# Kernel optimization log

Hardware: AMD Instinct MI355X
Metric: run time of the kernel (lower is better)

Reference implementation:

```python
import jax, jax.numpy as jnp
import numpy as np

B, T, I = 16384, 50, 5
H = 128
PRED_LEN = 12


def _uniform(key, shape, bound):
    return jax.random.uniform(key, shape, jnp.float32, -bound, bound)


def setup_inputs() -> dict:
    key = jax.random.key(0)
    ks = jax.random.split(key, 12)
    bound = 1.0 / np.sqrt(H)  # PyTorch LSTM/Linear default init
    return {
        "x": jax.random.normal(ks[0], (B, T, I), jnp.float32),
        "enc_Wih": _uniform(ks[1], (4 * H, I), bound),
        "enc_Whh": _uniform(ks[2], (4 * H, H), bound),
        "enc_bih": _uniform(ks[3], (4 * H,), bound),
        "enc_bhh": _uniform(ks[4], (4 * H,), bound),
        "dec_Wih": _uniform(ks[5], (4 * H, I), bound),
        "dec_Whh": _uniform(ks[6], (4 * H, H), bound),
        "dec_bih": _uniform(ks[7], (4 * H,), bound),
        "dec_bhh": _uniform(ks[8], (4 * H,), bound),
        "lin_W": _uniform(ks[9], (2, H), bound),
        "lin_b": _uniform(ks[10], (2,), bound),
    }


def _lstm_cell(x_t, h, c, Wih, Whh, bih, bhh):
    # PyTorch gate order: i, f, g, o
    gates = x_t @ Wih.T + h @ Whh.T + (bih + bhh)  # [B, 4H]
    i, f, g, o = jnp.split(gates, 4, axis=-1)
    i = jax.nn.sigmoid(i)
    f = jax.nn.sigmoid(f)
    g = jnp.tanh(g)
    o = jax.nn.sigmoid(o)
    c_new = f * c + i * g
    h_new = o * jnp.tanh(c_new)
    return h_new, c_new


def reference(x, enc_Wih, enc_Whh, enc_bih, enc_bhh,
              dec_Wih, dec_Whh, dec_bih, dec_bhh, lin_W, lin_b):
    b = x.shape[0]
    h0 = jnp.zeros((b, H), x.dtype)
    c0 = jnp.zeros((b, H), x.dtype)

    # ---- encoder LSTM over the history sequence ----
    def enc_step(carry, x_t):
        h, c = carry
        h, c = _lstm_cell(x_t, h, c, enc_Wih, enc_Whh, enc_bih, enc_bhh)
        return (h, c), None

    (h, c), _ = jax.lax.scan(enc_step, (h0, c0), jnp.swapaxes(x, 0, 1))

    static_context = x[:, -1, 2:]          # [B, I-2]
    last_velocity = x[:, -1, :2]           # [B, 2]
    dec_in0 = jnp.concatenate([last_velocity, static_context], axis=1)  # [B, I]

    def dec_step(carry, _):
        h, c, dec_in = carry
        h, c = _lstm_cell(dec_in, h, c, dec_Wih, dec_Whh, dec_bih, dec_bhh)
        pred = h @ lin_W.T + lin_b                      # [B, 2]
        dec_in = jnp.concatenate([pred, static_context], axis=1)
        return (h, c, dec_in), pred

    _, preds = jax.lax.scan(dec_step, (h, c, dec_in0), None, length=PRED_LEN)
    return jnp.swapaxes(preds, 0, 1)  # [B, pred_len, 2]
```

## Files before the change

kernel.cpp:

```cpp
#include <hip/hip_runtime.h>
#include <cstdint>

#define TT 50
#define II 5
#define PRED 12

typedef _Float16 f16;
typedef _Float16 f16x8 __attribute__((ext_vector_type(8)));
typedef float f32x4 __attribute__((ext_vector_type(4)));

__global__ void prep_weights(const float* __restrict__ Wih, const float* __restrict__ Whh,
                             const float* __restrict__ bih, const float* __restrict__ bhh,
                             f16* __restrict__ outw) {
    int f = blockIdx.x * 256 + threadIdx.x;
    if (f >= 81920) return;
    int j  = f & 7;
    int c  = (f >> 3) & 15;
    int q  = (f >> 7) & 3;
    int t2 = f >> 9;
    int kc = t2 % 5;
    int wg = t2 / 5;
    int w = wg >> 2, gsub = wg & 3;
    int g = gsub * 128 + w * 16 + c;
    int k = kc * 32 + q * 8 + j;
    float v;
    if (k < 128)       v = Whh[g * 128 + k];
    else if (k < 133)  v = Wih[g * 5 + (k - 128)];
    else if (k == 133) v = bih[g] + bhh[g];
    else               v = 0.f;
    outw[f] = (f16)v;
}

__device__ __forceinline__ float fsig(float x) {
    return __builtin_amdgcn_rcpf(1.f + __builtin_amdgcn_exp2f(-1.4426950408889634f * x));
}
__device__ __forceinline__ float ftanh(float x) {
    return 1.f - 2.f * __builtin_amdgcn_rcpf(1.f + __builtin_amdgcn_exp2f(2.885390081777927f * x));
}

__global__ __launch_bounds__(512, 2)
void lstm_kernel(const float* __restrict__ x,
                 const f16* __restrict__ wfrag,
                 const float* __restrict__ linW, const float* __restrict__ linB,
                 float* __restrict__ out) {
    __shared__ __align__(16) unsigned char state[64 * 512];
    __shared__ float predpart[8][64][2];

    const int tid  = threadIdx.x;
    const int lane = tid & 63;
    const int w    = tid >> 6;
    const int q    = lane >> 4;
    const int cl   = lane & 15;
    const int s0   = blockIdx.x * 64;
    const int jb   = w * 16 + q * 4;
    const int physh = ((jb >> 3) ^ (2 * cl)) & 31;
    const int hoff  = (jb & 7) * 2;

    f16x8 wr[4][5];
    {
        const f16x8* wp = (const f16x8*)wfrag;
        #pragma unroll
        for (int gs = 0; gs < 4; ++gs) {
            #pragma unroll
            for (int kc = 0; kc < 5; ++kc)
                wr[gs][kc] = wp[((w * 4 + gs) * 5 + kc) * 64 + lane];
        }
    }
    float w0r[4], w1r[4];
    #pragma unroll
    for (int idx = 0; idx < 4; ++idx) {
        w0r[idx] = linW[jb + idx];
        w1r[idx] = linW[128 + jb + idx];
    }
    float sc0 = 0.f, sc1 = 0.f, sc2 = 0.f;
    if (tid < 64) {
        const float* xr = x + (size_t)(s0 + tid) * (TT * II) + 49 * II;
        sc0 = xr[2]; sc1 = xr[3]; sc2 = xr[4];
    }
    {
        uint32_t* sp = (uint32_t*)state;
        #pragma unroll
        for (int r = 0; r < 16; ++r) sp[tid + r * 512] = 0u;
    }
    float creg[4][4];
    #pragma unroll
    for (int a = 0; a < 4; ++a)
        #pragma unroll
        for (int b = 0; b < 4; ++b) creg[a][b] = 0.f;

    __syncthreads();
    if (tid < 64) {
        const float* xr = x + (size_t)(s0 + tid) * (TT * II);
        union { f16 h[8]; uint4 u; } pk;
        pk.h[0] = (f16)xr[0]; pk.h[1] = (f16)xr[1]; pk.h[2] = (f16)xr[2];
        pk.h[3] = (f16)xr[3]; pk.h[4] = (f16)xr[4];
        pk.h[5] = (f16)1.f; pk.h[6] = (f16)0.f; pk.h[7] = (f16)0.f;
        int phys = 16 ^ (2 * (tid & 15));
        *(uint4*)(state + tid * 512 + phys * 16) = pk.u;
    }
    __syncthreads();

    f32x4 zero4 = {0.f, 0.f, 0.f, 0.f};

    #pragma unroll 1
    for (int t = 0; t < TT; ++t) {
        float xv0 = 0, xv1 = 0, xv2 = 0, xv3 = 0, xv4 = 0;
        if (tid < 64) {
            int tn = (t < TT - 1) ? t + 1 : TT - 1;
            const float* xr = x + (size_t)(s0 + tid) * (TT * II) + tn * II;
            xv0 = xr[0]; xv1 = xr[1]; xv2 = xr[2]; xv3 = xr[3]; xv4 = xr[4];
        }
        f32x4 acc[4][4];
        #pragma unroll
        for (int gs = 0; gs < 4; ++gs)
            #pragma unroll
            for (int ns = 0; ns < 4; ++ns) acc[gs][ns] = zero4;

        #pragma unroll
        for (int ns = 0; ns < 4; ++ns) {
            const int srow = ns * 16 + cl;
            #pragma unroll
            for (int kc = 0; kc < 5; ++kc) {
                const int phys = (kc * 4 + q) ^ (2 * cl);
                f16x8 bf = *(const f16x8*)(state + srow * 512 + phys * 16);
                acc[0][ns] = __builtin_amdgcn_mfma_f32_16x16x32_f16(wr[0][kc], bf, acc[0][ns], 0, 0, 0);
                acc[1][ns] = __builtin_amdgcn_mfma_f32_16x16x32_f16(wr[1][kc], bf, acc[1][ns], 0, 0, 0);
                acc[2][ns] = __builtin_amdgcn_mfma_f32_16x16x32_f16(wr[2][kc], bf, acc[2][ns], 0, 0, 0);
                acc[3][ns] = __builtin_amdgcn_mfma_f32_16x16x32_f16(wr[3][kc], bf, acc[3][ns], 0, 0, 0);
            }
        }
        uint2 hp[4];
        #pragma unroll
        for (int ns = 0; ns < 4; ++ns) {
            union { f16 h[4]; uint2 u; } pk;
            #pragma unroll
            for (int idx = 0; idx < 4; ++idx) {
                float ii = fsig(acc[0][ns][idx]);
                float ff = fsig(acc[1][ns][idx]);
                float gg = ftanh(acc[2][ns][idx]);
                float oo = fsig(acc[3][ns][idx]);
                float cn = ff * creg[ns][idx] + ii * gg;
                creg[ns][idx] = cn;
                pk.h[idx] = (f16)(oo * ftanh(cn));
            }
            hp[ns] = pk.u;
        }
        __syncthreads();
        #pragma unroll
        for (int ns = 0; ns < 4; ++ns)
            *(uint2*)(state + (ns * 16 + cl) * 512 + physh * 16 + hoff) = hp[ns];
        if (tid < 64) {
            union { f16 h[8]; uint4 u; } pk;
            pk.h[0] = (f16)xv0; pk.h[1] = (f16)xv1; pk.h[2] = (f16)xv2;
            pk.h[3] = (f16)xv3; pk.h[4] = (f16)xv4;
            pk.h[5] = (f16)1.f; pk.h[6] = (f16)0.f; pk.h[7] = (f16)0.f;
            int phys = 16 ^ (2 * (tid & 15));
            *(uint4*)(state + tid * 512 + phys * 16) = pk.u;
        }
        __syncthreads();
    }

    {
        const f16x8* wp = (const f16x8*)(wfrag + 81920);
        #pragma unroll
        for (int gs = 0; gs < 4; ++gs) {
            #pragma unroll
            for (int kc = 0; kc < 5; ++kc)
                wr[gs][kc] = wp[((w * 4 + gs) * 5 + kc) * 64 + lane];
        }
    }

    #pragma unroll 1
    for (int td = 0; td < PRED; ++td) {
        f32x4 acc[4][4];
        #pragma unroll
        for (int gs = 0; gs < 4; ++gs)
            #pragma unroll
            for (int ns = 0; ns < 4; ++ns) acc[gs][ns] = zero4;

        #pragma unroll
        for (int ns = 0; ns < 4; ++ns) {
            const int srow = ns * 16 + cl;
            #pragma unroll
            for (int kc = 0; kc < 5; ++kc) {
                const int phys = (kc * 4 + q) ^ (2 * cl);
                f16x8 bf = *(const f16x8*)(state + srow * 512 + phys * 16);
                acc[0][ns] = __builtin_amdgcn_mfma_f32_16x16x32_f16(wr[0][kc], bf, acc[0][ns], 0, 0, 0);
                acc[1][ns] = __builtin_amdgcn_mfma_f32_16x16x32_f16(wr[1][kc], bf, acc[1][ns], 0, 0, 0);
                acc[2][ns] = __builtin_amdgcn_mfma_f32_16x16x32_f16(wr[2][kc], bf, acc[2][ns], 0, 0, 0);
                acc[3][ns] = __builtin_amdgcn_mfma_f32_16x16x32_f16(wr[3][kc], bf, acc[3][ns], 0, 0, 0);
            }
        }
        uint2 hp[4];
        float p0[4], p1[4];
        #pragma unroll
        for (int ns = 0; ns < 4; ++ns) {
            union { f16 h[4]; uint2 u; } pk;
            p0[ns] = 0.f; p1[ns] = 0.f;
            #pragma unroll
            for (int idx = 0; idx < 4; ++idx) {
                float ii = fsig(acc[0][ns][idx]);
                float ff = fsig(acc[1][ns][idx]);
                float gg = ftanh(acc[2][ns][idx]);
                float oo = fsig(acc[3][ns][idx]);
                float cn = ff * creg[ns][idx] + ii * gg;
                creg[ns][idx] = cn;
                float hv = oo * ftanh(cn);
                p0[ns] += hv * w0r[idx];
                p1[ns] += hv * w1r[idx];
                pk.h[idx] = (f16)hv;
            }
            hp[ns] = pk.u;
        }
        #pragma unroll
        for (int ns = 0; ns < 4; ++ns) {
            p0[ns] += __shfl_xor(p0[ns], 16);
            p0[ns] += __shfl_xor(p0[ns], 32);
            p1[ns] += __shfl_xor(p1[ns], 16);
            p1[ns] += __shfl_xor(p1[ns], 32);
        }
        if (q == 0) {
            #pragma unroll
            for (int ns = 0; ns < 4; ++ns) {
                predpart[w][ns * 16 + cl][0] = p0[ns];
                predpart[w][ns * 16 + cl][1] = p1[ns];
            }
        }
        __syncthreads();
        #pragma unroll
        for (int ns = 0; ns < 4; ++ns)
            *(uint2*)(state + (ns * 16 + cl) * 512 + physh * 16 + hoff) = hp[ns];
        if (tid < 64) {
            float a0 = linB[0], a1 = linB[1];
            #pragma unroll
            for (int ww = 0; ww < 8; ++ww) {
                a0 += predpart[ww][tid][0];
                a1 += predpart[ww][tid][1];
            }
            float2 o2; o2.x = a0; o2.y = a1;
            *(float2*)(out + (size_t)(s0 + tid) * (PRED * 2) + td * 2) = o2;
            union { f16 h[8]; uint4 u; } pk;
            pk.h[0] = (f16)a0; pk.h[1] = (f16)a1;
            pk.h[2] = (f16)sc0; pk.h[3] = (f16)sc1; pk.h[4] = (f16)sc2;
            pk.h[5] = (f16)1.f; pk.h[6] = (f16)0.f; pk.h[7] = (f16)0.f;
            int phys = 16 ^ (2 * (tid & 15));
            *(uint4*)(state + tid * 512 + phys * 16) = pk.u;
        }
        __syncthreads();
    }
}

extern "C" void kernel_launch(void* const* d_in, const int* in_sizes, int n_in,
                              void* d_out, int out_size, void* d_ws, size_t ws_size,
                              hipStream_t stream) {
    (void)in_sizes; (void)n_in; (void)out_size; (void)ws_size;
    const float* x    = (const float*)d_in[0];
    const float* eWih = (const float*)d_in[1];
    const float* eWhh = (const float*)d_in[2];
    const float* ebih = (const float*)d_in[3];
    const float* ebhh = (const float*)d_in[4];
    const float* dWih = (const float*)d_in[5];
    const float* dWhh = (const float*)d_in[6];
    const float* dbih = (const float*)d_in[7];
    const float* dbhh = (const float*)d_in[8];
    const float* linW = (const float*)d_in[9];
    const float* linB = (const float*)d_in[10];
    f16* wfrag = (f16*)d_ws;

    prep_weights<<<320, 256, 0, stream>>>(eWih, eWhh, ebih, ebhh, wfrag);
    prep_weights<<<320, 256, 0, stream>>>(dWih, dWhh, dbih, dbhh, wfrag + 81920);
    lstm_kernel<<<256, 512, 0, stream>>>(x, wfrag, linW, linB, (float*)d_out);
}
```

Measured before the change: 279.5 us.

## Halve samples per block, double-buffer hidden state, stage x in LDS, drop prep kernels

Each block now handles 32 samples instead of 64 and the grid doubles to 512, with launch bounds raised to 4 blocks per CU, so more blocks can be resident across the device. The hidden state is double-buffered in LDS, which removes one barrier per timestep. All x inputs are staged as f16 in LDS up front instead of being loaded from global memory every step. The two weight-prep kernels are removed and each block converts the fp32 weights to f16 fragments itself, trading extra redundant global reads per block for fewer launches. The x/bias input chunk now goes through a separate MFMA operand, and the smaller per-block tile gives less weight reuse per block.

```diff
diff --git a/kernel.cpp b/kernel.cpp
--- a/kernel.cpp
+++ b/kernel.cpp
@@ -4,33 +4,13 @@
 #define TT 50
 #define II 5
 #define PRED 12
+#define SAMP 32
+#define NSB 2
 
 typedef _Float16 f16;
 typedef _Float16 f16x8 __attribute__((ext_vector_type(8)));
 typedef float f32x4 __attribute__((ext_vector_type(4)));
 
-__global__ void prep_weights(const float* __restrict__ Wih, const float* __restrict__ Whh,
-                             const float* __restrict__ bih, const float* __restrict__ bhh,
-                             f16* __restrict__ outw) {
-    int f = blockIdx.x * 256 + threadIdx.x;
-    if (f >= 81920) return;
-    int j  = f & 7;
-    int c  = (f >> 3) & 15;
-    int q  = (f >> 7) & 3;
-    int t2 = f >> 9;
-    int kc = t2 % 5;
-    int wg = t2 / 5;
-    int w = wg >> 2, gsub = wg & 3;
-    int g = gsub * 128 + w * 16 + c;
-    int k = kc * 32 + q * 8 + j;
-    float v;
-    if (k < 128)       v = Whh[g * 128 + k];
-    else if (k < 133)  v = Wih[g * 5 + (k - 128)];
-    else if (k == 133) v = bih[g] + bhh[g];
-    else               v = 0.f;
-    outw[f] = (f16)v;
-}
-
 __device__ __forceinline__ float fsig(float x) {
     return __builtin_amdgcn_rcpf(1.f + __builtin_amdgcn_exp2f(-1.4426950408889634f * x));
 }
@@ -38,200 +18,210 @@
     return 1.f - 2.f * __builtin_amdgcn_rcpf(1.f + __builtin_amdgcn_exp2f(2.885390081777927f * x));
 }
 
-__global__ __launch_bounds__(512, 2)
+__device__ __forceinline__ void load_frags(const float* __restrict__ Wih,
+                                           const float* __restrict__ Whh,
+                                           const float* __restrict__ bih,
+                                           const float* __restrict__ bhh,
+                                           int w, int q, int cl, f16x8 wr[4][5]) {
+    #pragma unroll
+    for (int gs = 0; gs < 4; ++gs) {
+        const int g = gs * 128 + w * 16 + cl;
+        const float* whr = Whh + g * 128 + q * 8;
+        #pragma unroll
+        for (int kc = 0; kc < 4; ++kc) {
+            f32x4 a = *(const f32x4*)(whr + kc * 32);
+            f32x4 b = *(const f32x4*)(whr + kc * 32 + 4);
+            f16x8 f;
+            f[0] = (f16)a[0]; f[1] = (f16)a[1]; f[2] = (f16)a[2]; f[3] = (f16)a[3];
+            f[4] = (f16)b[0]; f[5] = (f16)b[1]; f[6] = (f16)b[2]; f[7] = (f16)b[3];
+            wr[gs][kc] = f;
+        }
+        f16x8 f;
+        #pragma unroll
+        for (int j = 0; j < 8; ++j) f[j] = (f16)0.f;
+        if (q == 0) {
+            f[0] = (f16)Wih[g * 5 + 0]; f[1] = (f16)Wih[g * 5 + 1];
+            f[2] = (f16)Wih[g * 5 + 2]; f[3] = (f16)Wih[g * 5 + 3];
+            f[4] = (f16)Wih[g * 5 + 4];
+            f[5] = (f16)(bih[g] + bhh[g]);
+        }
+        wr[gs][4] = f;
+    }
+}
+
+__global__ __launch_bounds__(512, 4)
 void lstm_kernel(const float* __restrict__ x,
-                 const f16* __restrict__ wfrag,
+                 const float* __restrict__ eWih, const float* __restrict__ eWhh,
+                 const float* __restrict__ ebih, const float* __restrict__ ebhh,
+                 const float* __restrict__ dWih, const float* __restrict__ dWhh,
+                 const float* __restrict__ dbih, const float* __restrict__ dbhh,
                  const float* __restrict__ linW, const float* __restrict__ linB,
                  float* __restrict__ out) {
-    __shared__ __align__(16) unsigned char state[64 * 512];
-    __shared__ float predpart[8][64][2];
+    __shared__ __align__(16) unsigned char state[2 * SAMP * 256];
+    __shared__ __align__(16) f16 xstage[52 * SAMP * 8];
+    __shared__ float predpart[8][SAMP][2];
 
     const int tid  = threadIdx.x;
     const int lane = tid & 63;
     const int w    = tid >> 6;
     const int q    = lane >> 4;
     const int cl   = lane & 15;
-    const int s0   = blockIdx.x * 64;
+    const int s0   = blockIdx.x * SAMP;
     const int jb   = w * 16 + q * 4;
-    const int physh = ((jb >> 3) ^ (2 * cl)) & 31;
+    const int physh = ((jb >> 3) ^ (2 * (cl & 7))) & 15;
     const int hoff  = (jb & 7) * 2;
 
+    int hro[4];
+    #pragma unroll
+    for (int kc = 0; kc < 4; ++kc)
+        hro[kc] = cl * 256 + ((((kc * 4 + q) ^ (2 * (cl & 7))) & 15) << 4);
+    const int hwo = cl * 256 + physh * 16 + hoff;
+
+    {
+        uint32_t* sp = (uint32_t*)state;
+        #pragma unroll
+        for (int r = 0; r < 8; ++r) sp[tid + r * 512] = 0u;
+    }
+    #pragma unroll
+    for (int k = 0; k < 4; ++k) {
+        int c = tid + k * 512;
+        if (c < TT * SAMP) {
+            int t = c >> 5, s = c & 31;
+            const float* xr = x + (size_t)(s0 + s) * (TT * II) + t * II;
+            union { f16 h[8]; uint4 u; } pk;
+            pk.h[0] = (f16)xr[0]; pk.h[1] = (f16)xr[1]; pk.h[2] = (f16)xr[2];
+            pk.h[3] = (f16)xr[3]; pk.h[4] = (f16)xr[4];
+            pk.h[5] = (f16)1.f;  pk.h[6] = (f16)0.f;  pk.h[7] = (f16)0.f;
+            *(uint4*)(xstage + (t * SAMP + s) * 8) = pk.u;
+        }
+    }
+
     f16x8 wr[4][5];
-    {
-        const f16x8* wp = (const f16x8*)wfrag;
-        #pragma unroll
-        for (int gs = 0; gs < 4; ++gs) {
-            #pragma unroll
-            for (int kc = 0; kc < 5; ++kc)
-                wr[gs][kc] = wp[((w * 4 + gs) * 5 + kc) * 64 + lane];
-        }
-    }
+    load_frags(eWih, eWhh, ebih, ebhh, w, q, cl, wr);
+
+    float creg[NSB][4];
+    #pragma unroll
+    for (int ns = 0; ns < NSB; ++ns)
+        #pragma unroll
+        for (int i = 0; i < 4; ++i) creg[ns][i] = 0.f;
+
+    const f32x4 zero4 = {0.f, 0.f, 0.f, 0.f};
+    __syncthreads();
+
+    #pragma unroll 1
+    for (int t = 0; t < TT; ++t) {
+        const int curoff = (t & 1) << 13;
+        const int nxtoff = curoff ^ 8192;
+        #pragma unroll
+        for (int ns = 0; ns < NSB; ++ns) {
+            const unsigned char* cb = state + curoff + ns * 4096;
+            f16x8 bx = *(const f16x8*)(xstage + (t * SAMP + ns * 16 + cl) * 8);
+            f16x8 b0 = *(const f16x8*)(cb + hro[0]);
+            f32x4 a0 = __builtin_amdgcn_mfma_f32_16x16x32_f16(wr[0][0], b0, zero4, 0, 0, 0);
+            f32x4 a1 = __builtin_amdgcn_mfma_f32_16x16x32_f16(wr[1][0], b0, zero4, 0, 0, 0);
+            f32x4 a2 = __builtin_amdgcn_mfma_f32_16x16x32_f16(wr[2][0], b0, zero4, 0, 0, 0);
+            f32x4 a3 = __builtin_amdgcn_mfma_f32_16x16x32_f16(wr[3][0], b0, zero4, 0, 0, 0);
+            #pragma unroll
+            for (int kc = 1; kc < 4; ++kc) {
+                f16x8 bh = *(const f16x8*)(cb + hro[kc]);
+                a0 = __builtin_amdgcn_mfma_f32_16x16x32_f16(wr[0][kc], bh, a0, 0, 0, 0);
+                a1 = __builtin_amdgcn_mfma_f32_16x16x32_f16(wr[1][kc], bh, a1, 0, 0, 0);
+                a2 = __builtin_amdgcn_mfma_f32_16x16x32_f16(wr[2][kc], bh, a2, 0, 0, 0);
+                a3 = __builtin_amdgcn_mfma_f32_16x16x32_f16(wr[3][kc], bh, a3, 0, 0, 0);
+            }
+            a0 = __builtin_amdgcn_mfma_f32_16x16x32_f16(wr[0][4], bx, a0, 0, 0, 0);
+            a1 = __builtin_amdgcn_mfma_f32_16x16x32_f16(wr[1][4], bx, a1, 0, 0, 0);
+            a2 = __builtin_amdgcn_mfma_f32_16x16x32_f16(wr[2][4], bx, a2, 0, 0, 0);
+            a3 = __builtin_amdgcn_mfma_f32_16x16x32_f16(wr[3][4], bx, a3, 0, 0, 0);
+
+            union { f16 h[4]; uint2 u; } pk;
+            #pragma unroll
+            for (int idx = 0; idx < 4; ++idx) {
+                float ii = fsig(a0[idx]);
+                float ff = fsig(a1[idx]);
+                float gg = ftanh(a2[idx]);
+                float oo = fsig(a3[idx]);
+                float cn = ff * creg[ns][idx] + ii * gg;
+                creg[ns][idx] = cn;
+                pk.h[idx] = (f16)(oo * ftanh(cn));
+            }
+            *(uint2*)(state + nxtoff + ns * 4096 + hwo) = pk.u;
+        }
+        __syncthreads();
+    }
+
+    load_frags(dWih, dWhh, dbih, dbhh, w, q, cl, wr);
     float w0r[4], w1r[4];
     #pragma unroll
     for (int idx = 0; idx < 4; ++idx) {
         w0r[idx] = linW[jb + idx];
         w1r[idx] = linW[128 + jb + idx];
     }
-    float sc0 = 0.f, sc1 = 0.f, sc2 = 0.f;
-    if (tid < 64) {
+    float sc0 = 0.f, sc1 = 0.f, sc2 = 0.f, lb0 = 0.f, lb1 = 0.f;
+    if (tid < SAMP) {
         const float* xr = x + (size_t)(s0 + tid) * (TT * II) + 49 * II;
         sc0 = xr[2]; sc1 = xr[3]; sc2 = xr[4];
-    }
-    {
-        uint32_t* sp = (uint32_t*)state;
-        #pragma unroll
-        for (int r = 0; r < 16; ++r) sp[tid + r * 512] = 0u;
-    }
-    float creg[4][4];
-    #pragma unroll
-    for (int a = 0; a < 4; ++a)
-        #pragma unroll
-        for (int b = 0; b < 4; ++b) creg[a][b] = 0.f;
-
-    __syncthreads();
-    if (tid < 64) {
-        const float* xr = x + (size_t)(s0 + tid) * (TT * II);
-        union { f16 h[8]; uint4 u; } pk;
-        pk.h[0] = (f16)xr[0]; pk.h[1] = (f16)xr[1]; pk.h[2] = (f16)xr[2];
-        pk.h[3] = (f16)xr[3]; pk.h[4] = (f16)xr[4];
-        pk.h[5] = (f16)1.f; pk.h[6] = (f16)0.f; pk.h[7] = (f16)0.f;
-        int phys = 16 ^ (2 * (tid & 15));
-        *(uint4*)(state + tid * 512 + phys * 16) = pk.u;
-    }
-    __syncthreads();
-
-    f32x4 zero4 = {0.f, 0.f, 0.f, 0.f};
-
-    #pragma unroll 1
-    for (int t = 0; t < TT; ++t) {
-        float xv0 = 0, xv1 = 0, xv2 = 0, xv3 = 0, xv4 = 0;
-        if (tid < 64) {
-            int tn = (t < TT - 1) ? t + 1 : TT - 1;
-            const float* xr = x + (size_t)(s0 + tid) * (TT * II) + tn * II;
-            xv0 = xr[0]; xv1 = xr[1]; xv2 = xr[2]; xv3 = xr[3]; xv4 = xr[4];
-        }
-        f32x4 acc[4][4];
-        #pragma unroll
-        for (int gs = 0; gs < 4; ++gs)
-            #pragma unroll
-            for (int ns = 0; ns < 4; ++ns) acc[gs][ns] = zero4;
-
-        #pragma unroll
-        for (int ns = 0; ns < 4; ++ns) {
-            const int srow = ns * 16 + cl;
-            #pragma unroll
-            for (int kc = 0; kc < 5; ++kc) {
-                const int phys = (kc * 4 + q) ^ (2 * cl);
-                f16x8 bf = *(const f16x8*)(state + srow * 512 + phys * 16);
-                acc[0][ns] = __builtin_amdgcn_mfma_f32_16x16x32_f16(wr[0][kc], bf, acc[0][ns], 0, 0, 0);
-                acc[1][ns] = __builtin_amdgcn_mfma_f32_16x16x32_f16(wr[1][kc], bf, acc[1][ns], 0, 0, 0);
-                acc[2][ns] = __builtin_amdgcn_mfma_f32_16x16x32_f16(wr[2][kc], bf, acc[2][ns], 0, 0, 0);
-                acc[3][ns] = __builtin_amdgcn_mfma_f32_16x16x32_f16(wr[3][kc], bf, acc[3][ns], 0, 0, 0);
-            }
-        }
-        uint2 hp[4];
-        #pragma unroll
-        for (int ns = 0; ns < 4; ++ns) {
-            union { f16 h[4]; uint2 u; } pk;
-            #pragma unroll
-            for (int idx = 0; idx < 4; ++idx) {
-                float ii = fsig(acc[0][ns][idx]);
-                float ff = fsig(acc[1][ns][idx]);
-                float gg = ftanh(acc[2][ns][idx]);
-                float oo = fsig(acc[3][ns][idx]);
-                float cn = ff * creg[ns][idx] + ii * gg;
-                creg[ns][idx] = cn;
-                pk.h[idx] = (f16)(oo * ftanh(cn));
-            }
-            hp[ns] = pk.u;
-        }
-        __syncthreads();
-        #pragma unroll
-        for (int ns = 0; ns < 4; ++ns)
-            *(uint2*)(state + (ns * 16 + cl) * 512 + physh * 16 + hoff) = hp[ns];
-        if (tid < 64) {
-            union { f16 h[8]; uint4 u; } pk;
-            pk.h[0] = (f16)xv0; pk.h[1] = (f16)xv1; pk.h[2] = (f16)xv2;
-            pk.h[3] = (f16)xv3; pk.h[4] = (f16)xv4;
-            pk.h[5] = (f16)1.f; pk.h[6] = (f16)0.f; pk.h[7] = (f16)0.f;
-            int phys = 16 ^ (2 * (tid & 15));
-            *(uint4*)(state + tid * 512 + phys * 16) = pk.u;
-        }
-        __syncthreads();
-    }
-
-    {
-        const f16x8* wp = (const f16x8*)(wfrag + 81920);
-        #pragma unroll
-        for (int gs = 0; gs < 4; ++gs) {
-            #pragma unroll
-            for (int kc = 0; kc < 5; ++kc)
-                wr[gs][kc] = wp[((w * 4 + gs) * 5 + kc) * 64 + lane];
-        }
+        lb0 = linB[0]; lb1 = linB[1];
     }
 
     #pragma unroll 1
     for (int td = 0; td < PRED; ++td) {
-        f32x4 acc[4][4];
-        #pragma unroll
-        for (int gs = 0; gs < 4; ++gs)
-            #pragma unroll
-            for (int ns = 0; ns < 4; ++ns) acc[gs][ns] = zero4;
-
-        #pragma unroll
-        for (int ns = 0; ns < 4; ++ns) {
-            const int srow = ns * 16 + cl;
-            #pragma unroll
-            for (int kc = 0; kc < 5; ++kc) {
-                const int phys = (kc * 4 + q) ^ (2 * cl);
-                f16x8 bf = *(const f16x8*)(state + srow * 512 + phys * 16);
-                acc[0][ns] = __builtin_amdgcn_mfma_f32_16x16x32_f16(wr[0][kc], bf, acc[0][ns], 0, 0, 0);
-                acc[1][ns] = __builtin_amdgcn_mfma_f32_16x16x32_f16(wr[1][kc], bf, acc[1][ns], 0, 0, 0);
-                acc[2][ns] = __builtin_amdgcn_mfma_f32_16x16x32_f16(wr[2][kc], bf, acc[2][ns], 0, 0, 0);
-                acc[3][ns] = __builtin_amdgcn_mfma_f32_16x16x32_f16(wr[3][kc], bf, acc[3][ns], 0, 0, 0);
-            }
-        }
-        uint2 hp[4];
-        float p0[4], p1[4];
-        #pragma unroll
-        for (int ns = 0; ns < 4; ++ns) {
+        const int curoff = (td & 1) << 13;
+        const int nxtoff = curoff ^ 8192;
+        const int xslot  = (td == 0) ? 49 : (50 + (td & 1));
+        float p0s[NSB], p1s[NSB];
+        #pragma unroll
+        for (int ns = 0; ns < NSB; ++ns) {
+            const unsigned char* cb = state + curoff + ns * 4096;
+            f16x8 bx = *(const f16x8*)(xstage + (xslot * SAMP + ns * 16 + cl) * 8);
+            f16x8 b0 = *(const f16x8*)(cb + hro[0]);
+            f32x4 a0 = __builtin_amdgcn_mfma_f32_16x16x32_f16(wr[0][0], b0, zero4, 0, 0, 0);
+            f32x4 a1 = __builtin_amdgcn_mfma_f32_16x16x32_f16(wr[1][0], b0, zero4, 0, 0, 0);
+            f32x4 a2 = __builtin_amdgcn_mfma_f32_16x16x32_f16(wr[2][0], b0, zero4, 0, 0, 0);
+            f32x4 a3 = __builtin_amdgcn_mfma_f32_16x16x32_f16(wr[3][0], b0, zero4, 0, 0, 0);
+            #pragma unroll
+            for (int kc = 1; kc < 4; ++kc) {
+                f16x8 bh = *(const f16x8*)(cb + hro[kc]);
+                a0 = __builtin_amdgcn_mfma_f32_16x16x32_f16(wr[0][kc], bh, a0, 0, 0, 0);
+                a1 = __builtin_amdgcn_mfma_f32_16x16x32_f16(wr[1][kc], bh, a1, 0, 0, 0);
+                a2 = __builtin_amdgcn_mfma_f32_16x16x32_f16(wr[2][kc], bh, a2, 0, 0, 0);
+                a3 = __builtin_amdgcn_mfma_f32_16x16x32_f16(wr[3][kc], bh, a3, 0, 0, 0);
+            }
+            a0 = __builtin_amdgcn_mfma_f32_16x16x32_f16(wr[0][4], bx, a0, 0, 0, 0);
+            a1 = __builtin_amdgcn_mfma_f32_16x16x32_f16(wr[1][4], bx, a1, 0, 0, 0);
+            a2 = __builtin_amdgcn_mfma_f32_16x16x32_f16(wr[2][4], bx, a2, 0, 0, 0);
+            a3 = __builtin_amdgcn_mfma_f32_16x16x32_f16(wr[3][4], bx, a3, 0, 0, 0);
+
+            float p0 = 0.f, p1 = 0.f;
             union { f16 h[4]; uint2 u; } pk;
-            p0[ns] = 0.f; p1[ns] = 0.f;
             #pragma unroll
             for (int idx = 0; idx < 4; ++idx) {
-                float ii = fsig(acc[0][ns][idx]);
-                float ff = fsig(acc[1][ns][idx]);
-                float gg = ftanh(acc[2][ns][idx]);
-                float oo = fsig(acc[3][ns][idx]);
+                float ii = fsig(a0[idx]);
+                float ff = fsig(a1[idx]);
+                float gg = ftanh(a2[idx]);
+                float oo = fsig(a3[idx]);
                 float cn = ff * creg[ns][idx] + ii * gg;
                 creg[ns][idx] = cn;
                 float hv = oo * ftanh(cn);
-                p0[ns] += hv * w0r[idx];
-                p1[ns] += hv * w1r[idx];
+                p0 += hv * w0r[idx];
+                p1 += hv * w1r[idx];
                 pk.h[idx] = (f16)hv;
             }
-            hp[ns] = pk.u;
-        }
-        #pragma unroll
-        for (int ns = 0; ns < 4; ++ns) {
-            p0[ns] += __shfl_xor(p0[ns], 16);
-            p0[ns] += __shfl_xor(p0[ns], 32);
-            p1[ns] += __shfl_xor(p1[ns], 16);
-            p1[ns] += __shfl_xor(p1[ns], 32);
+            *(uint2*)(state + nxtoff + ns * 4096 + hwo) = pk.u;
+            p0 += __shfl_xor(p0, 16); p0 += __shfl_xor(p0, 32);
+            p1 += __shfl_xor(p1, 16); p1 += __shfl_xor(p1, 32);
+            p0s[ns] = p0; p1s[ns] = p1;
         }
         if (q == 0) {
             #pragma unroll
-            for (int ns = 0; ns < 4; ++ns) {
-                predpart[w][ns * 16 + cl][0] = p0[ns];
-                predpart[w][ns * 16 + cl][1] = p1[ns];
+            for (int ns = 0; ns < NSB; ++ns) {
+                predpart[w][ns * 16 + cl][0] = p0s[ns];
+                predpart[w][ns * 16 + cl][1] = p1s[ns];
             }
         }
         __syncthreads();
-        #pragma unroll
-        for (int ns = 0; ns < 4; ++ns)
-            *(uint2*)(state + (ns * 16 + cl) * 512 + physh * 16 + hoff) = hp[ns];
-        if (tid < 64) {
-            float a0 = linB[0], a1 = linB[1];
+        if (tid < SAMP) {
+            float a0 = lb0, a1 = lb1;
             #pragma unroll
             for (int ww = 0; ww < 8; ++ww) {
                 a0 += predpart[ww][tid][0];
@@ -240,11 +230,11 @@
             float2 o2; o2.x = a0; o2.y = a1;
             *(float2*)(out + (size_t)(s0 + tid) * (PRED * 2) + td * 2) = o2;
             union { f16 h[8]; uint4 u; } pk;
-            pk.h[0] = (f16)a0; pk.h[1] = (f16)a1;
+            pk.h[0] = (f16)a0;  pk.h[1] = (f16)a1;
             pk.h[2] = (f16)sc0; pk.h[3] = (f16)sc1; pk.h[4] = (f16)sc2;
             pk.h[5] = (f16)1.f; pk.h[6] = (f16)0.f; pk.h[7] = (f16)0.f;
-            int phys = 16 ^ (2 * (tid & 15));
-            *(uint4*)(state + tid * 512 + phys * 16) = pk.u;
+            int ws = 50 + ((td + 1) & 1);
+            *(uint4*)(xstage + (ws * SAMP + tid) * 8) = pk.u;
         }
         __syncthreads();
     }
@@ -253,7 +243,7 @@
 extern "C" void kernel_launch(void* const* d_in, const int* in_sizes, int n_in,
                               void* d_out, int out_size, void* d_ws, size_t ws_size,
                               hipStream_t stream) {
-    (void)in_sizes; (void)n_in; (void)out_size; (void)ws_size;
+    (void)in_sizes; (void)n_in; (void)out_size; (void)d_ws; (void)ws_size;
     const float* x    = (const float*)d_in[0];
     const float* eWih = (const float*)d_in[1];
     const float* eWhh = (const float*)d_in[2];
@@ -265,9 +255,8 @@
     const float* dbhh = (const float*)d_in[8];
     const float* linW = (const float*)d_in[9];
     const float* linB = (const float*)d_in[10];
-    f16* wfrag = (f16*)d_ws;
-
-    prep_weights<<<320, 256, 0, stream>>>(eWih, eWhh, ebih, ebhh, wfrag);
-    prep_weights<<<320, 256, 0, stream>>>(dWih, dWhh, dbih, dbhh, wfrag + 81920);
-    lstm_kernel<<<256, 512, 0, stream>>>(x, wfrag, linW, linB, (float*)d_out);
-}
+
+    lstm_kernel<<<512, 512, 0, stream>>>(x, eWih, eWhh, ebih, ebhh,
+                                         dWih, dWhh, dbih, dbhh,
+                                         linW, linB, (float*)d_out);
+}
```

Measured after the change: 412.5 us. 47.6% more time.
